# Kernel tuning notes

Measured on AMD Instinct MI355X. Metric: run time of the kernel, lower is better.

The kernel has to match this reference:

```python
import jax, jax.numpy as jnp
import numpy as np
import math

B, N, D_MODEL, D_QK, D_V = 8, 2048, 512, 64, 64
NEG_INF = float('-inf')

def setup_inputs() -> dict:
    key = jax.random.key(0)
    k1, k2, k3, k4, k5 = jax.random.split(key, 5)
    mask = jax.random.randint(k1, (B, N, N), 0, 2).astype(bool)
    x_key_value = jax.random.normal(k2, (B, N, D_MODEL), dtype=jnp.float32)
    wk = jax.random.normal(k3, (D_MODEL, D_QK), dtype=jnp.float32) * 0.02
    wq = jax.random.normal(k4, (D_MODEL, D_QK), dtype=jnp.float32) * 0.02
    wv = jax.random.normal(k5, (D_MODEL, D_V), dtype=jnp.float32) * 0.02
    return {"mask": mask, "x_key_value": x_key_value, "wk": wk, "wq": wq, "wv": wv}

def reference(mask, x_key_value, wk, wq, wv):
    # self-attention: x_query defaults to x_key_value
    div = math.sqrt(wk.shape[1])
    k = x_key_value @ wk          # [n, j, d_qk]
    q = x_key_value @ wq          # [n, i, d_qk]
    v = x_key_value @ wv          # [n, j, d_v]
    mat = jnp.einsum('nik,njk->nij', q, k) / div
    mat = jnp.where(mask, mat, NEG_INF)
    portion = jax.nn.softmax(mat, axis=2)
    return jnp.einsum('nij,njk->nik', portion, v)
```

## Files before the change

kernel.cpp:

```cpp
#include <hip/hip_runtime.h>
#include <hip/hip_bf16.h>

typedef __attribute__((ext_vector_type(8))) short bf16x8;
typedef __attribute__((ext_vector_type(4))) float f32x4;
typedef __hip_bfloat16 bf16;
typedef unsigned long long ull;

#define BATCH 8
#define SEQ   2048
#define DMODEL 512
#define DHEAD 64
#define ROWS (BATCH * SEQ)
#define SCALE_LOG2 0.1803368801f

static __device__ inline short f2bf(float f) {
    union { __hip_bfloat16 h; short s; } u;
    u.h = __float2bfloat16(f);
    return u.s;
}

__global__ __launch_bounds__(256) void pack_mask_kernel(
    const int* __restrict__ mask, ull* __restrict__ pm)
{
    const int wgl = (blockIdx.x * 256 + threadIdx.x) >> 6;
    const int lane = threadIdx.x & 63;
    const uint4* src = (const uint4*)mask;
    const size_t cbase = (size_t)wgl * 32;

    for (int it = 0; it < 8; ++it) {
        size_t c0 = cbase + it * 4;
        uint4 v0 = src[(c0 + 0) * 64 + lane];
        uint4 v1 = src[(c0 + 1) * 64 + lane];
        uint4 v2 = src[(c0 + 2) * 64 + lane];
        uint4 v3 = src[(c0 + 3) * 64 + lane];
        ull b00 = __ballot(v0.x != 0), b01 = __ballot(v0.y != 0);
        ull b02 = __ballot(v0.z != 0), b03 = __ballot(v0.w != 0);
        ull b10 = __ballot(v1.x != 0), b11 = __ballot(v1.y != 0);
        ull b12 = __ballot(v1.z != 0), b13 = __ballot(v1.w != 0);
        ull b20 = __ballot(v2.x != 0), b21 = __ballot(v2.y != 0);
        ull b22 = __ballot(v2.z != 0), b23 = __ballot(v2.w != 0);
        ull b30 = __ballot(v3.x != 0), b31 = __ballot(v3.y != 0);
        ull b32 = __ballot(v3.z != 0), b33 = __ballot(v3.w != 0);
        if (lane == 0) {
            ull* d = pm + c0 * 4;
            d[0] = b00; d[1] = b01; d[2]  = b02; d[3]  = b03;
            d[4] = b10; d[5] = b11; d[6]  = b12; d[7]  = b13;
            d[8] = b20; d[9] = b21; d[10] = b22; d[11] = b23;
            d[12] = b30; d[13] = b31; d[14] = b32; d[15] = b33;
        }
    }
}

__global__ __launch_bounds__(256) void transpose_w_kernel(
    const float* __restrict__ wq, const float* __restrict__ wk,
    const float* __restrict__ wv, bf16* __restrict__ wt)
{
    const int s  = blockIdx.x / 8;
    const int kt = blockIdx.x % 8;
    const float* w = (s == 0) ? wq : ((s == 1) ? wk : wv);

    __shared__ float Ts[64][68];

    const int tid = threadIdx.x;
    int nr = tid >> 4;
    int n4 = (tid & 15) * 4;
#pragma unroll
    for (int p = 0; p < 4; ++p) {
        int k = 16 * p + nr;
        float4 v = *(const float4*)(w + (size_t)(kt * 64 + k) * DHEAD + n4);
        Ts[k][n4] = v.x; Ts[k][n4 + 1] = v.y; Ts[k][n4 + 2] = v.z; Ts[k][n4 + 3] = v.w;
    }
    __syncthreads();
#pragma unroll
    for (int p = 0; p < 2; ++p) {
        int cc = tid + p * 256;
        int n = cc >> 3;
        int kk = (cc & 7) * 8;
        bf16x8 o;
#pragma unroll
        for (int e = 0; e < 8; ++e) o[e] = f2bf(Ts[kk + e][n]);
        *(bf16x8*)(wt + (size_t)(s * 64 + n) * DMODEL + kt * 64 + kk) = o;
    }
}

__global__ __launch_bounds__(512, 4) void proj_kernel(
    const float* __restrict__ x, const bf16* __restrict__ wt,
    bf16* __restrict__ Q, bf16* __restrict__ K, bf16* __restrict__ Vt)
{
    const int bb = blockIdx.x & 7;
    const int tt = blockIdx.x >> 3;
    const int r0 = bb * SEQ + tt * 32;
    const int tid = threadIdx.x;
    const int lane = tid & 63;
    const int wid = tid >> 6;
    const int strip = wid & 1;
    const int cq = wid >> 1;
    const int l15 = lane & 15;
    const int quad = lane >> 4;

    __shared__ __align__(8) bf16 Vs[64][36];

    f32x4 acc[3] = {};

    const float* xp = x + (size_t)(r0 + 16 * strip + l15) * DMODEL + quad * 8;

    float4 A0[4], A1[4];
    A0[0] = *(const float4*)(xp + 0);  A0[1] = *(const float4*)(xp + 4);
    A0[2] = *(const float4*)(xp + 32); A0[3] = *(const float4*)(xp + 36);
    A1[0] = *(const float4*)(xp + 64); A1[1] = *(const float4*)(xp + 68);
    A1[2] = *(const float4*)(xp + 96); A1[3] = *(const float4*)(xp + 100);

#pragma unroll
    for (int k0 = 0; k0 < DMODEL; k0 += 64) {
        float4* cur = ((k0 >> 6) & 1) ? A1 : A0;
        bf16x8 a0, a1;
        a0[0] = f2bf(cur[0].x); a0[1] = f2bf(cur[0].y); a0[2] = f2bf(cur[0].z); a0[3] = f2bf(cur[0].w);
        a0[4] = f2bf(cur[1].x); a0[5] = f2bf(cur[1].y); a0[6] = f2bf(cur[1].z); a0[7] = f2bf(cur[1].w);
        a1[0] = f2bf(cur[2].x); a1[1] = f2bf(cur[2].y); a1[2] = f2bf(cur[2].z); a1[3] = f2bf(cur[2].w);
        a1[4] = f2bf(cur[3].x); a1[5] = f2bf(cur[3].y); a1[6] = f2bf(cur[3].z); a1[7] = f2bf(cur[3].w);

        if (k0 + 128 < DMODEL) {
            cur[0] = *(const float4*)(xp + k0 + 128);
            cur[1] = *(const float4*)(xp + k0 + 132);
            cur[2] = *(const float4*)(xp + k0 + 160);
            cur[3] = *(const float4*)(xp + k0 + 164);
        }

#pragma unroll
        for (int g = 0; g < 3; ++g) {
            int n = 16 * (3 * cq + g) + l15;
            const bf16* wp = wt + (size_t)n * DMODEL + k0 + quad * 8;
            bf16x8 b0 = *(const bf16x8*)(wp);
            bf16x8 b1 = *(const bf16x8*)(wp + 32);
            acc[g] = __builtin_amdgcn_mfma_f32_16x16x32_bf16(a0, b0, acc[g], 0, 0, 0);
            acc[g] = __builtin_amdgcn_mfma_f32_16x16x32_bf16(a1, b1, acc[g], 0, 0, 0);
        }
    }

#pragma unroll
    for (int g = 0; g < 3; ++g) {
        int ng = 16 * (3 * cq + g) + l15;
        int sel = ng >> 6;
        int col = ng & 63;
#pragma unroll
        for (int r = 0; r < 4; ++r) {
            int rowl = 16 * strip + quad * 4 + r;
            int row = r0 + rowl;
            union { __hip_bfloat16 h; bf16 b; } u;
            u.h = __float2bfloat16(acc[g][r]);
            if (sel == 0)      Q[(size_t)row * DHEAD + col] = u.b;
            else if (sel == 1) K[(size_t)row * DHEAD + col] = u.b;
            else               Vs[col][rowl] = u.b;
        }
    }
    __syncthreads();

    {
        int d = tid >> 3;
        int j4 = (tid & 7) * 4;
        int j0 = tt * 32;
        uint2 payload = *(const uint2*)(&Vs[d][j4]);
        *(uint2*)(Vt + ((size_t)(bb * DHEAD + d)) * SEQ + j0 + j4) = payload;
    }
}

__global__ __launch_bounds__(256, 4) void flash_kernel(
    const bf16* __restrict__ Q, const bf16* __restrict__ K,
    const bf16* __restrict__ Vt, const ull* __restrict__ pm,
    float* __restrict__ out)
{
    const int b = blockIdx.x;
    const int q0 = blockIdx.y * 16;
    const int tid = threadIdx.x;
    const int lane = tid & 63;
    const int wid = tid >> 6;
    const int l15 = lane & 15;
    const int quad = lane >> 4;

    __shared__ __align__(16) bf16 Ps[4][16][72];
    __shared__ float Om[4][16][64];
    __shared__ float Lw[4][16];

    ull mw[2][4];
    {
        const int sh = l15 >> 2;
#pragma unroll
        for (int ch = 0; ch < 2; ++ch)
#pragma unroll
            for (int r = 0; r < 4; ++r) {
                size_t row = (size_t)(b * SEQ + q0 + quad * 4 + r);
                mw[ch][r] = pm[(row * 8 + wid * 2 + ch) * 4 + (l15 & 3)] >> sh;
            }
    }

    const bf16* qp = Q + ((size_t)(b * SEQ + q0 + l15)) * DHEAD + quad * 8;
    bf16x8 aQ0 = *(const bf16x8*)(qp);
    bf16x8 aQ1 = *(const bf16x8*)(qp + 32);

    f32x4 oacc[4] = {};
    float lsum[4] = {0.f, 0.f, 0.f, 0.f};

    const int jbase = wid * (SEQ / 4);

#pragma unroll
    for (int jt = 0; jt < 8; ++jt) {
        const int ch = jt >> 2;
        const int s = jt & 3;
        const int j0 = jbase + jt * 64;

        f32x4 sacc[4] = {};
#pragma unroll
        for (int c = 0; c < 4; ++c) {
            const bf16* kp = K + ((size_t)(b * SEQ + j0 + 16 * c + l15)) * DHEAD + quad * 8;
            bf16x8 b0 = *(const bf16x8*)(kp);
            bf16x8 b1 = *(const bf16x8*)(kp + 32);
            sacc[c] = __builtin_amdgcn_mfma_f32_16x16x32_bf16(aQ0, b0, sacc[c], 0, 0, 0);
            sacc[c] = __builtin_amdgcn_mfma_f32_16x16x32_bf16(aQ1, b1, sacc[c], 0, 0, 0);
        }

        float pv[4][4];
#pragma unroll
        for (int c = 0; c < 4; ++c)
#pragma unroll
            for (int r = 0; r < 4; ++r) {
                float e = exp2f(sacc[c][r] * SCALE_LOG2);
                unsigned bit = (unsigned)(mw[ch][r] >> (16 * s + 4 * c)) & 1u;
                float p = bit ? e : 0.0f;
                pv[c][r] = p;
                lsum[r] += p;
            }

#pragma unroll
        for (int c = 0; c < 4; ++c)
#pragma unroll
            for (int r = 0; r < 4; ++r) {
                union { __hip_bfloat16 h; bf16 b; } u;
                u.h = __float2bfloat16(pv[c][r]);
                Ps[wid][quad * 4 + r][16 * c + l15] = u.b;
            }

        bf16x8 aP0 = *(const bf16x8*)(&Ps[wid][l15][quad * 8]);
        bf16x8 aP1 = *(const bf16x8*)(&Ps[wid][l15][32 + quad * 8]);
#pragma unroll
        for (int c = 0; c < 4; ++c) {
            const bf16* vp = Vt + ((size_t)b * DHEAD + 16 * c + l15) * SEQ + j0 + quad * 8;
            bf16x8 v0 = *(const bf16x8*)(vp);
            bf16x8 v1 = *(const bf16x8*)(vp + 32);
            oacc[c] = __builtin_amdgcn_mfma_f32_16x16x32_bf16(aP0, v0, oacc[c], 0, 0, 0);
            oacc[c] = __builtin_amdgcn_mfma_f32_16x16x32_bf16(aP1, v1, oacc[c], 0, 0, 0);
        }
    }

#pragma unroll
    for (int r = 0; r < 4; ++r) {
        lsum[r] += __shfl_xor(lsum[r], 1);
        lsum[r] += __shfl_xor(lsum[r], 2);
        lsum[r] += __shfl_xor(lsum[r], 4);
        lsum[r] += __shfl_xor(lsum[r], 8);
    }

#pragma unroll
    for (int c = 0; c < 4; ++c)
#pragma unroll
        for (int r = 0; r < 4; ++r)
            Om[wid][quad * 4 + r][16 * c + l15] = oacc[c][r];
    if (l15 == 0) {
#pragma unroll
        for (int r = 0; r < 4; ++r) Lw[wid][quad * 4 + r] = lsum[r];
    }
    __syncthreads();

    {
        int row = tid >> 4;
        int c0 = (tid & 15) * 4;
        float L = Lw[0][row] + Lw[1][row] + Lw[2][row] + Lw[3][row];
        float invL = 1.0f / L;
        float4 o;
        float* op = (float*)&o;
#pragma unroll
        for (int e = 0; e < 4; ++e) {
            op[e] = (Om[0][row][c0 + e] + Om[1][row][c0 + e] +
                     Om[2][row][c0 + e] + Om[3][row][c0 + e]) * invL;
        }
        *(float4*)(out + ((size_t)(b * SEQ + q0 + row)) * DHEAD + c0) = o;
    }
}

extern "C" void kernel_launch(void* const* d_in, const int* in_sizes, int n_in,
                              void* d_out, int out_size, void* d_ws, size_t ws_size,
                              hipStream_t stream)
{
    const int*   mask = (const int*)d_in[0];
    const float* x    = (const float*)d_in[1];
    const float* wk   = (const float*)d_in[2];
    const float* wq   = (const float*)d_in[3];
    const float* wv   = (const float*)d_in[4];
    float* out = (float*)d_out;

    bf16* Qb = (bf16*)d_ws;
    bf16* Kb = Qb + (size_t)ROWS * DHEAD;
    bf16* Vt = Kb + (size_t)ROWS * DHEAD;
    bf16* Wt = Vt + (size_t)BATCH * DHEAD * SEQ;
    ull*  pm = (ull*)(Wt + 3 * 64 * DMODEL);

    pack_mask_kernel<<<dim3(1024), 256, 0, stream>>>(mask, pm);
    transpose_w_kernel<<<dim3(24), 256, 0, stream>>>(wq, wk, wv, Wt);
    proj_kernel<<<dim3(ROWS / 32), 512, 0, stream>>>(x, Wt, Qb, Kb, Vt);
    flash_kernel<<<dim3(BATCH, SEQ / 16), 256, 0, stream>>>(Qb, Kb, Vt, pm, out);
}
```

Before: 322.5 us.

## Shrink per-block work in mask pack and projection, load mask words per tile

The mask packer now runs twice as many blocks with half the loop trip count. The projection kernel drops to 256 threads covering 16 rows per block, with no register double-buffering of x loads. The flash kernel drops the occupancy hint from launch bounds, loads mask words inside the loop instead of keeping 8 ull in registers, and fuses the exp/mask step with the bf16 store to shared memory. Together these aim to cut register pressure and raise occupancy and parallelism, at the cost of less latency hiding for the x loads and extra mask loads per iteration.

New measurement: 313.3 us. -2.8%, faster.

```diff
diff --git a/kernel.cpp b/kernel.cpp
--- a/kernel.cpp
+++ b/kernel.cpp
@@ -25,9 +25,9 @@
     const int wgl = (blockIdx.x * 256 + threadIdx.x) >> 6;
     const int lane = threadIdx.x & 63;
     const uint4* src = (const uint4*)mask;
-    const size_t cbase = (size_t)wgl * 32;
-
-    for (int it = 0; it < 8; ++it) {
+    const size_t cbase = (size_t)wgl * 16;
+
+    for (int it = 0; it < 4; ++it) {
         size_t c0 = cbase + it * 4;
         uint4 v0 = src[(c0 + 0) * 64 + lane];
         uint4 v1 = src[(c0 + 1) * 64 + lane];
@@ -83,48 +83,36 @@
     }
 }
 
-__global__ __launch_bounds__(512, 4) void proj_kernel(
+__global__ __launch_bounds__(256) void proj_kernel(
     const float* __restrict__ x, const bf16* __restrict__ wt,
     bf16* __restrict__ Q, bf16* __restrict__ K, bf16* __restrict__ Vt)
 {
     const int bb = blockIdx.x & 7;
     const int tt = blockIdx.x >> 3;
-    const int r0 = bb * SEQ + tt * 32;
+    const int r0 = bb * SEQ + tt * 16;
     const int tid = threadIdx.x;
     const int lane = tid & 63;
-    const int wid = tid >> 6;
-    const int strip = wid & 1;
-    const int cq = wid >> 1;
+    const int cq = tid >> 6;
     const int l15 = lane & 15;
     const int quad = lane >> 4;
 
-    __shared__ __align__(8) bf16 Vs[64][36];
+    __shared__ __align__(8) bf16 Vs[64][20];
 
     f32x4 acc[3] = {};
 
-    const float* xp = x + (size_t)(r0 + 16 * strip + l15) * DMODEL + quad * 8;
-
-    float4 A0[4], A1[4];
-    A0[0] = *(const float4*)(xp + 0);  A0[1] = *(const float4*)(xp + 4);
-    A0[2] = *(const float4*)(xp + 32); A0[3] = *(const float4*)(xp + 36);
-    A1[0] = *(const float4*)(xp + 64); A1[1] = *(const float4*)(xp + 68);
-    A1[2] = *(const float4*)(xp + 96); A1[3] = *(const float4*)(xp + 100);
+    const float* xp = x + (size_t)(r0 + l15) * DMODEL + quad * 8;
 
 #pragma unroll
     for (int k0 = 0; k0 < DMODEL; k0 += 64) {
-        float4* cur = ((k0 >> 6) & 1) ? A1 : A0;
+        float4 xa = *(const float4*)(xp + k0);
+        float4 xb = *(const float4*)(xp + k0 + 4);
+        float4 xc = *(const float4*)(xp + k0 + 32);
+        float4 xd = *(const float4*)(xp + k0 + 36);
         bf16x8 a0, a1;
-        a0[0] = f2bf(cur[0].x); a0[1] = f2bf(cur[0].y); a0[2] = f2bf(cur[0].z); a0[3] = f2bf(cur[0].w);
-        a0[4] = f2bf(cur[1].x); a0[5] = f2bf(cur[1].y); a0[6] = f2bf(cur[1].z); a0[7] = f2bf(cur[1].w);
-        a1[0] = f2bf(cur[2].x); a1[1] = f2bf(cur[2].y); a1[2] = f2bf(cur[2].z); a1[3] = f2bf(cur[2].w);
-        a1[4] = f2bf(cur[3].x); a1[5] = f2bf(cur[3].y); a1[6] = f2bf(cur[3].z); a1[7] = f2bf(cur[3].w);
-
-        if (k0 + 128 < DMODEL) {
-            cur[0] = *(const float4*)(xp + k0 + 128);
-            cur[1] = *(const float4*)(xp + k0 + 132);
-            cur[2] = *(const float4*)(xp + k0 + 160);
-            cur[3] = *(const float4*)(xp + k0 + 164);
-        }
+        a0[0] = f2bf(xa.x); a0[1] = f2bf(xa.y); a0[2] = f2bf(xa.z); a0[3] = f2bf(xa.w);
+        a0[4] = f2bf(xb.x); a0[5] = f2bf(xb.y); a0[6] = f2bf(xb.z); a0[7] = f2bf(xb.w);
+        a1[0] = f2bf(xc.x); a1[1] = f2bf(xc.y); a1[2] = f2bf(xc.z); a1[3] = f2bf(xc.w);
+        a1[4] = f2bf(xd.x); a1[5] = f2bf(xd.y); a1[6] = f2bf(xd.z); a1[7] = f2bf(xd.w);
 
 #pragma unroll
         for (int g = 0; g < 3; ++g) {
@@ -144,7 +132,7 @@
         int col = ng & 63;
 #pragma unroll
         for (int r = 0; r < 4; ++r) {
-            int rowl = 16 * strip + quad * 4 + r;
+            int rowl = quad * 4 + r;
             int row = r0 + rowl;
             union { __hip_bfloat16 h; bf16 b; } u;
             u.h = __float2bfloat16(acc[g][r]);
@@ -156,15 +144,14 @@
     __syncthreads();
 
     {
-        int d = tid >> 3;
-        int j4 = (tid & 7) * 4;
-        int j0 = tt * 32;
+        int d = tid >> 2;
+        int j4 = (tid & 3) * 4;
         uint2 payload = *(const uint2*)(&Vs[d][j4]);
-        *(uint2*)(Vt + ((size_t)(bb * DHEAD + d)) * SEQ + j0 + j4) = payload;
-    }
-}
-
-__global__ __launch_bounds__(256, 4) void flash_kernel(
+        *(uint2*)(Vt + ((size_t)(bb * DHEAD + d)) * SEQ + tt * 16 + j4) = payload;
+    }
+}
+
+__global__ __launch_bounds__(256) void flash_kernel(
     const bf16* __restrict__ Q, const bf16* __restrict__ K,
     const bf16* __restrict__ Vt, const ull* __restrict__ pm,
     float* __restrict__ out)
@@ -181,17 +168,11 @@
     __shared__ float Om[4][16][64];
     __shared__ float Lw[4][16];
 
-    ull mw[2][4];
-    {
-        const int sh = l15 >> 2;
-#pragma unroll
-        for (int ch = 0; ch < 2; ++ch)
-#pragma unroll
-            for (int r = 0; r < 4; ++r) {
-                size_t row = (size_t)(b * SEQ + q0 + quad * 4 + r);
-                mw[ch][r] = pm[(row * 8 + wid * 2 + ch) * 4 + (l15 & 3)] >> sh;
-            }
-    }
+    const int sh = l15 >> 2;
+    const ull* p0 = pm + ((size_t)(b * SEQ + q0 + quad * 4 + 0) * 8 + wid * 2) * 4 + (l15 & 3);
+    const ull* p1 = pm + ((size_t)(b * SEQ + q0 + quad * 4 + 1) * 8 + wid * 2) * 4 + (l15 & 3);
+    const ull* p2 = pm + ((size_t)(b * SEQ + q0 + quad * 4 + 2) * 8 + wid * 2) * 4 + (l15 & 3);
+    const ull* p3 = pm + ((size_t)(b * SEQ + q0 + quad * 4 + 3) * 8 + wid * 2) * 4 + (l15 & 3);
 
     const bf16* qp = Q + ((size_t)(b * SEQ + q0 + l15)) * DHEAD + quad * 8;
     bf16x8 aQ0 = *(const bf16x8*)(qp);
@@ -207,6 +188,11 @@
         const int ch = jt >> 2;
         const int s = jt & 3;
         const int j0 = jbase + jt * 64;
+
+        ull w0 = p0[ch * 4] >> sh;
+        ull w1 = p1[ch * 4] >> sh;
+        ull w2 = p2[ch * 4] >> sh;
+        ull w3 = p3[ch * 4] >> sh;
 
         f32x4 sacc[4] = {};
 #pragma unroll
@@ -218,26 +204,37 @@
             sacc[c] = __builtin_amdgcn_mfma_f32_16x16x32_bf16(aQ1, b1, sacc[c], 0, 0, 0);
         }
 
-        float pv[4][4];
-#pragma unroll
-        for (int c = 0; c < 4; ++c)
-#pragma unroll
-            for (int r = 0; r < 4; ++r) {
-                float e = exp2f(sacc[c][r] * SCALE_LOG2);
-                unsigned bit = (unsigned)(mw[ch][r] >> (16 * s + 4 * c)) & 1u;
-                float p = bit ? e : 0.0f;
-                pv[c][r] = p;
-                lsum[r] += p;
+#pragma unroll
+        for (int c = 0; c < 4; ++c) {
+            {
+                float e = exp2f(sacc[c][0] * SCALE_LOG2);
+                float p = ((w0 >> (16 * s + 4 * c)) & 1ull) ? e : 0.0f;
+                lsum[0] += p;
+                union { __hip_bfloat16 h; bf16 b; } u; u.h = __float2bfloat16(p);
+                Ps[wid][quad * 4 + 0][16 * c + l15] = u.b;
             }
-
-#pragma unroll
-        for (int c = 0; c < 4; ++c)
-#pragma unroll
-            for (int r = 0; r < 4; ++r) {
-                union { __hip_bfloat16 h; bf16 b; } u;
-                u.h = __float2bfloat16(pv[c][r]);
-                Ps[wid][quad * 4 + r][16 * c + l15] = u.b;
+            {
+                float e = exp2f(sacc[c][1] * SCALE_LOG2);
+                float p = ((w1 >> (16 * s + 4 * c)) & 1ull) ? e : 0.0f;
+                lsum[1] += p;
+                union { __hip_bfloat16 h; bf16 b; } u; u.h = __float2bfloat16(p);
+                Ps[wid][quad * 4 + 1][16 * c + l15] = u.b;
             }
+            {
+                float e = exp2f(sacc[c][2] * SCALE_LOG2);
+                float p = ((w2 >> (16 * s + 4 * c)) & 1ull) ? e : 0.0f;
+                lsum[2] += p;
+                union { __hip_bfloat16 h; bf16 b; } u; u.h = __float2bfloat16(p);
+                Ps[wid][quad * 4 + 2][16 * c + l15] = u.b;
+            }
+            {
+                float e = exp2f(sacc[c][3] * SCALE_LOG2);
+                float p = ((w3 >> (16 * s + 4 * c)) & 1ull) ? e : 0.0f;
+                lsum[3] += p;
+                union { __hip_bfloat16 h; bf16 b; } u; u.h = __float2bfloat16(p);
+                Ps[wid][quad * 4 + 3][16 * c + l15] = u.b;
+            }
+        }
 
         bf16x8 aP0 = *(const bf16x8*)(&Ps[wid][l15][quad * 8]);
         bf16x8 aP1 = *(const bf16x8*)(&Ps[wid][l15][32 + quad * 8]);
@@ -303,8 +300,8 @@
     bf16* Wt = Vt + (size_t)BATCH * DHEAD * SEQ;
     ull*  pm = (ull*)(Wt + 3 * 64 * DMODEL);
 
-    pack_mask_kernel<<<dim3(1024), 256, 0, stream>>>(mask, pm);
+    pack_mask_kernel<<<dim3(2048), 256, 0, stream>>>(mask, pm);
     transpose_w_kernel<<<dim3(24), 256, 0, stream>>>(wq, wk, wv, Wt);
-    proj_kernel<<<dim3(ROWS / 32), 512, 0, stream>>>(x, Wt, Qb, Kb, Vt);
+    proj_kernel<<<dim3(1024), 256, 0, stream>>>(x, Wt, Qb, Kb, Vt);
     flash_kernel<<<dim3(BATCH, SEQ / 16), 256, 0, stream>>>(Qb, Kb, Vt, pm, out);
 }
```
